# Optimization experiments

Hardware: AMD Instinct MI355X
Metric: run time of the kernel (lower is better)

## Reference

```python
import jax, jax.numpy as jnp
import numpy as np
import math

# config (mirrors FastAttentionConfig)
D_MODEL = 512
D_KEY = 64      # == d_query (required by AbsorptionProjection shape algebra)
D_QUERY = 64
N_HEADS = 8
RANK = 32
RFF_DIM = 128
K_MAX = 64
DIM_GROUPS = [8] * 8  # hyper_cuts_dim_groups, sums to D_KEY
B, L = 2, 2048


def setup_inputs() -> dict:
    key = jax.random.key(0)
    ks = jax.random.split(key, 16)
    r = lambda k, shape, s=1.0: jax.random.normal(k, shape, dtype=jnp.float32) * s
    isr = 1.0 / math.sqrt(RANK)
    return {
        "query": r(ks[0], (B, L, D_MODEL)),
        "key":   r(ks[1], (B, L, D_MODEL)),
        "value": r(ks[2], (B, L, D_MODEL)),
        # down projections (nn.Linear weights stored as (in, out))
        "Wq":  r(ks[3], (D_MODEL, D_QUERY), 0.02), "bq": jnp.zeros((D_QUERY,), jnp.float32),
        "Wkv": r(ks[4], (D_MODEL, D_KEY), 0.02),   "bkv": jnp.zeros((D_KEY,), jnp.float32),
        # per-head absorption projection factors
        "u_q": r(ks[5], (N_HEADS, D_QUERY, RANK), isr), "v_q": r(ks[6], (N_HEADS, RANK, D_KEY), isr),
        "u_k": r(ks[7], (N_HEADS, D_KEY, RANK), isr),   "v_k": r(ks[8], (N_HEADS, RANK, D_KEY), isr),
        # per-head low-rank value up-projection
        "u_v": r(ks[9], (N_HEADS, D_KEY, RANK), isr),   "v_v": r(ks[10], (N_HEADS, RANK, D_MODEL), isr),
        # per-head random Fourier features (frozen params)
        "omega": r(ks[11], (N_HEADS, D_KEY, RFF_DIM)),
        "rff_bias": jax.random.uniform(ks[12], (N_HEADS, RFF_DIM), jnp.float32) * (2.0 * math.pi),
        # output projection
        "W_out": r(ks[13], (N_HEADS * D_MODEL, D_MODEL), 0.02),
        "b_out": jnp.zeros((D_MODEL,), jnp.float32),
    }


def _group_codes(x):
    """Binary-quantize each hyper-cuts dim group and pack bits into one int code per group."""
    codes, start = [], 0
    for gd in DIM_GROUPS:
        bits = (x[..., start:start + gd] > 0).astype(jnp.int32)
        pw = (2 ** jnp.arange(gd, dtype=jnp.int32))
        codes.append(jnp.sum(bits * pw, axis=-1))  # (B, L) int32
        start += gd
    return codes


def _candidates(Qp, K):
    """Wu-Manber prefix match AND Trie full match == exact binary-code match per group
    (prefix_len == group dim). Per group keep first K_MAX matches (ascending index),
    union across groups, sorted ascending, -1-padding handled via mask."""
    Bq, Lq, _ = Qp.shape
    qc, kc = _group_codes(Qp), _group_codes(K)
    union = jnp.zeros((Bq, Lq, Lq), bool)
    for cq, ck in zip(qc, kc):
        m = cq[:, :, None] == ck[:, None, :]                       # (B, L, L)
        keep = m & (jnp.cumsum(m.astype(jnp.int32), axis=-1) <= K_MAX)
        union = union | keep
    idx = jnp.where(union, jnp.arange(Lq, dtype=jnp.int32)[None, None, :], Lq)
    cand = jnp.sort(idx, axis=-1)[:, :, :K_MAX]                    # (B, L, K_MAX)
    mask = cand < Lq
    return jnp.where(mask, cand, 0), mask


def reference(query, key, value, Wq, bq, Wkv, bkv, u_q, v_q, u_k, v_k,
              u_v, v_v, omega, rff_bias, W_out, b_out):
    q_down = query @ Wq + bq          # (B, L, D_QUERY)
    k_down = key @ Wkv + bkv          # (B, L, D_KEY)
    v_down = value @ Wkv + bkv        # (B, L, D_KEY)
    rff_scale = math.sqrt(2.0 / RFF_DIM)
    inv_sqrt = 1.0 / math.sqrt(RFF_DIM)  # optimized_sqrt(RFF_DIM), RFF_DIM is 2^k
    heads = []
    for h in range(N_HEADS):
        # absorption projection: Q into key space
        W_UQ = u_q[h] @ v_q[h]                 # (D_QUERY, D_KEY)
        W_UK = u_k[h] @ v_k[h]                 # (D_KEY, D_KEY)
        W_absorb = W_UK.T @ W_UQ               # (D_KEY, D_QUERY)
        Qp = q_down @ W_absorb.T               # (B, L, D_KEY)
        cand, mask = _candidates(Qp, k_down)
        # RFF-kernelized scores, gathered at candidate positions
        phi_q = jnp.cos(Qp @ omega[h] + rff_bias[h]) * rff_scale     # (B, L, R)
        phi_k = jnp.cos(k_down @ omega[h] + rff_bias[h]) * rff_scale
        scores = jnp.einsum('bir,bjr->bij', phi_q, phi_k) * inv_sqrt  # (B, L, L)
        s = jnp.take_along_axis(scores, cand, axis=2)                 # (B, L, K_MAX)
        s = jnp.where(mask, s, -1e30)
        w = jax.nn.softmax(s, axis=-1) * mask                         # zero invalid slots
        # gather candidate values (d_key space), weighted sum, then low-rank up-proj
        Vc = jnp.take_along_axis(v_down[:, None, :, :], cand[..., None], axis=2)  # (B,L,K,dk)
        ctx = jnp.einsum('blk,blkd->bld', w, Vc)                      # (B, L, D_KEY)
        heads.append(ctx @ (u_v[h] @ v_v[h]))                         # (B, L, D_MODEL)
    concat = jnp.concatenate(heads, axis=-1)                          # (B, L, H*D_MODEL)
    return concat @ W_out + b_out                                     # dropout: eval mode
```

## Files before the change

### kernel.cpp

```cpp
#include <hip/hip_runtime.h>
#include <hip/hip_bf16.h>
#include <math.h>

#define BB 2
#define LL 2048
#define DM 512
#define DK 64
#define NH 8
#define RK 32
#define RFF 128
#define KMAX 64
#define BL (BB*LL)
#define NQ (NH*BB*LL)
#define NCH 16
#define CHW (LL/NCH)

#define RFF_SCALE 0.125f
#define INV_SQRT_RFF 0.08838834764831845f

typedef unsigned long long u64;

__device__ __forceinline__ unsigned int zbytes(unsigned int x) {
  return ~(((x & 0x7F7F7F7Fu) + 0x7F7F7F7Fu) | x | 0x7F7F7F7Fu);
}

__global__ __launch_bounds__(256) void k_down_proj(
    const float* __restrict__ q, const float* __restrict__ k, const float* __restrict__ v,
    const float* __restrict__ Wq, const float* __restrict__ bq,
    const float* __restrict__ Wkv, const float* __restrict__ bkv,
    float* __restrict__ qd, float* __restrict__ kd, float* __restrict__ vd,
    unsigned char* __restrict__ kcodes) {
  int r0 = blockIdx.x * 16;
  int which = blockIdx.y;
  const float* src = (which == 0) ? q : (which == 1) ? k : v;
  const float* W   = (which == 0) ? Wq : Wkv;
  const float* bias= (which == 0) ? bq : bkv;
  float* dst       = (which == 0) ? qd : (which == 1) ? kd : vd;
  int tid = threadIdx.x;
  int d = tid & 63, rg = tid >> 6;

  __shared__ float sin_[16][DM];
  const float4* s4 = (const float4*)(src + (size_t)r0 * DM);
  float4* l4 = (float4*)&sin_[0][0];
  #pragma unroll
  for (int u = 0; u < 8; ++u) l4[tid + u * 256] = s4[tid + u * 256];
  __syncthreads();

  float acc[4] = {0.f, 0.f, 0.f, 0.f};
  for (int t4 = 0; t4 < DM / 4; ++t4) {
    float w[4];
    #pragma unroll
    for (int u = 0; u < 4; ++u) w[u] = W[(t4 * 4 + u) * DK + d];
    #pragma unroll
    for (int r = 0; r < 4; ++r) {
      float4 c4 = *(const float4*)&sin_[rg * 4 + r][t4 * 4];
      acc[r] = fmaf(c4.x, w[0], acc[r]);
      acc[r] = fmaf(c4.y, w[1], acc[r]);
      acc[r] = fmaf(c4.z, w[2], acc[r]);
      acc[r] = fmaf(c4.w, w[3], acc[r]);
    }
  }
  float bs = bias[d];
  #pragma unroll
  for (int r = 0; r < 4; ++r) {
    int R = r0 + rg * 4 + r;
    float val = acc[r] + bs;
    dst[(size_t)R * DK + d] = val;
    if (which == 1) {
      u64 m = __ballot(val > 0.f);
      if (d < 8) {
        int b = R >> 11, j = R & 2047;
        kcodes[(((size_t)b * 8 + d) << 11) + j] = (unsigned char)((m >> (8 * d)) & 0xFF);
      }
    }
  }
}

__global__ __launch_bounds__(256) void k_head_pre(
    const float* __restrict__ u_q, const float* __restrict__ v_q,
    const float* __restrict__ u_k, const float* __restrict__ v_k,
    const float* __restrict__ u_v, const float* __restrict__ v_v,
    float* __restrict__ WabsT, float* __restrict__ Wv) {
  int h = blockIdx.x, tid = threadIdx.x;
  __shared__ float sU[DK * RK];
  __shared__ float sV[RK * DK];
  __shared__ float sWUQ[DK * DK];
  __shared__ float sWUK[DK * DK];
  for (int e = tid; e < DK * RK; e += 256) sU[e] = u_q[h * DK * RK + e];
  for (int e = tid; e < RK * DK; e += 256) sV[e] = v_q[h * RK * DK + e];
  __syncthreads();
  for (int e = tid; e < DK * DK; e += 256) {
    int r = e >> 6, c = e & 63;
    float a = 0.f;
    for (int t = 0; t < RK; ++t) a = fmaf(sU[r * RK + t], sV[t * DK + c], a);
    sWUQ[e] = a;
  }
  __syncthreads();
  for (int e = tid; e < DK * RK; e += 256) sU[e] = u_k[h * DK * RK + e];
  for (int e = tid; e < RK * DK; e += 256) sV[e] = v_k[h * RK * DK + e];
  __syncthreads();
  for (int e = tid; e < DK * DK; e += 256) {
    int r = e >> 6, c = e & 63;
    float a = 0.f;
    for (int t = 0; t < RK; ++t) a = fmaf(sU[r * RK + t], sV[t * DK + c], a);
    sWUK[e] = a;
  }
  __syncthreads();
  for (int e = tid; e < DK * DK; e += 256) {
    int a_ = e >> 6, q_ = e & 63;
    float a = 0.f;
    for (int c = 0; c < DK; ++c) a = fmaf(sWUK[c * DK + a_], sWUQ[c * DK + q_], a);
    WabsT[h * DK * DK + q_ * DK + a_] = a;
  }
  __syncthreads();
  for (int e = tid; e < DK * RK; e += 256) sU[e] = u_v[h * DK * RK + e];
  __syncthreads();
  const float* vv = v_v + (size_t)h * RK * DM;
  for (int e = tid; e < DK * DM; e += 256) {
    int d = e >> 9, o = e & 511;
    float a = 0.f;
    for (int c = 0; c < RK; ++c) a = fmaf(sU[d * RK + c], vv[c * DM + o], a);
    Wv[(size_t)h * DK * DM + e] = a;
  }
}

__global__ __launch_bounds__(256) void k_m2(
    const float* __restrict__ Wv, const float* __restrict__ W_out, float* __restrict__ M2) {
  int h = blockIdx.x, d0 = blockIdx.y * 8;
  int tid = threadIdx.x;
  __shared__ float4 sWv4[8][DM / 4];
  const float4* g4 = (const float4*)(Wv + ((size_t)h * DK + d0) * DM);
  float4* l4 = &sWv4[0][0];
  #pragma unroll
  for (int u = 0; u < 4; ++u) l4[tid + u * 256] = g4[tid + u * 256];
  __syncthreads();
  float a0[8], a1[8];
  #pragma unroll
  for (int r = 0; r < 8; ++r) { a0[r] = 0.f; a1[r] = 0.f; }
  const float* Wo = W_out + (size_t)h * DM * DM;
  for (int p4 = 0; p4 < DM / 4; ++p4) {
    float m0[4], m1[4];
    #pragma unroll
    for (int u = 0; u < 4; ++u) {
      m0[u] = Wo[(size_t)(p4 * 4 + u) * DM + tid];
      m1[u] = Wo[(size_t)(p4 * 4 + u) * DM + tid + 256];
    }
    #pragma unroll
    for (int r = 0; r < 8; ++r) {
      float4 c4 = sWv4[r][p4];
      a0[r] = fmaf(c4.x, m0[0], a0[r]); a0[r] = fmaf(c4.y, m0[1], a0[r]);
      a0[r] = fmaf(c4.z, m0[2], a0[r]); a0[r] = fmaf(c4.w, m0[3], a0[r]);
      a1[r] = fmaf(c4.x, m1[0], a1[r]); a1[r] = fmaf(c4.y, m1[1], a1[r]);
      a1[r] = fmaf(c4.z, m1[2], a1[r]); a1[r] = fmaf(c4.w, m1[3], a1[r]);
    }
  }
  #pragma unroll
  for (int r = 0; r < 8; ++r) {
    size_t row = (size_t)h * DK + d0 + r;
    M2[row * DM + tid] = a0[r];
    M2[row * DM + tid + 256] = a1[r];
  }
}

__global__ __launch_bounds__(256, 4) void k_phi(
    const float* __restrict__ qd, const float* __restrict__ kd,
    const float* __restrict__ WabsT,
    const float* __restrict__ omega, const float* __restrict__ rff_bias,
    float* __restrict__ phiq, float* __restrict__ phik,
    u64* __restrict__ qcodes8) {
  int r0 = blockIdx.x * 16;
  int h = blockIdx.y;
  int isK = blockIdx.z;
  int tid = threadIdx.x;
  __shared__ float sq[16][DK];
  __shared__ float qp[16][DK];

  if (!isK) {
    const float4* g4 = (const float4*)(qd + (size_t)r0 * DK);
    float4* l4 = (float4*)&sq[0][0];
    l4[tid] = g4[tid];
    __syncthreads();
    int a_ = tid & 63, rg = tid >> 6;
    float acc[4] = {0.f, 0.f, 0.f, 0.f};
    const float* Wt = WabsT + h * DK * DK;
    for (int t = 0; t < DK; ++t) {
      float w = Wt[t * DK + a_];
      #pragma unroll
      for (int r = 0; r < 4; ++r) acc[r] = fmaf(sq[rg * 4 + r][t], w, acc[r]);
    }
    #pragma unroll
    for (int r = 0; r < 4; ++r) {
      u64 m = __ballot(acc[r] > 0.f);
      int R = r0 + rg * 4 + r;
      if (a_ == 0) {
        int b = R >> 11, i = R & 2047;
        qcodes8[(((size_t)h * BB + b) << 11) + i] = m;
      }
      qp[R - r0][a_] = acc[r];
    }
    __syncthreads();
  } else {
    const float4* g4 = (const float4*)(kd + (size_t)r0 * DK);
    float4* l4 = (float4*)&qp[0][0];
    l4[tid] = g4[tid];
    __syncthreads();
  }

  int col = tid & 127, rg2 = tid >> 7;
  float acc[8];
  float bias = rff_bias[h * RFF + col];
  #pragma unroll
  for (int r = 0; r < 8; ++r) acc[r] = bias;
  const float* om = omega + (size_t)h * DK * RFF;
  #pragma unroll 4
  for (int d4 = 0; d4 < DK / 4; ++d4) {
    float w[4];
    #pragma unroll
    for (int u = 0; u < 4; ++u) w[u] = om[(size_t)(d4 * 4 + u) * RFF + col];
    #pragma unroll
    for (int r = 0; r < 8; ++r) {
      float4 c4 = *(const float4*)&qp[rg2 * 8 + r][d4 * 4];
      acc[r] = fmaf(c4.x, w[0], acc[r]); acc[r] = fmaf(c4.y, w[1], acc[r]);
      acc[r] = fmaf(c4.z, w[2], acc[r]); acc[r] = fmaf(c4.w, w[3], acc[r]);
    }
  }
  float* dst = isK ? phik : phiq;
  #pragma unroll
  for (int r = 0; r < 8; ++r) {
    int R = r0 + rg2 * 8 + r;
    dst[((size_t)h * BL + R) * RFF + col] = cosf(acc[r]) * RFF_SCALE;
  }
}

__global__ __launch_bounds__(256) void k_bhist(
    const unsigned char* __restrict__ kcodes, int* __restrict__ chist) {
  int bg = blockIdx.x, ch = blockIdx.y;
  int c = threadIdx.x;
  __shared__ unsigned int wrd[CHW / 4];
  if (c < CHW / 4)
    wrd[c] = ((const unsigned int*)(kcodes + (size_t)bg * LL + ch * CHW))[c];
  __syncthreads();
  unsigned int pat = (unsigned)c * 0x01010101u;
  int cnt = 0;
  #pragma unroll
  for (int t = 0; t < CHW / 4; ++t)
    cnt += __popc(zbytes(wrd[t] ^ pat));
  chist[((size_t)bg * NCH + ch) * 256 + c] = cnt;
}

__global__ __launch_bounds__(256) void k_bscan(
    int* __restrict__ chist, int* __restrict__ bcnt) {
  int bg = blockIdx.x, c = threadIdx.x;
  int base = 0;
  #pragma unroll
  for (int ch = 0; ch < NCH; ++ch) {
    size_t idx = ((size_t)bg * NCH + ch) * 256 + c;
    int v = chist[idx];
    chist[idx] = base;
    base += v;
  }
  bcnt[bg * 256 + c] = base < KMAX ? base : KMAX;
}

__global__ __launch_bounds__(256) void k_bscatter(
    const unsigned char* __restrict__ kcodes, const int* __restrict__ chist,
    int* __restrict__ bidx) {
  int bg = blockIdx.x, ch = blockIdx.y;
  int c = threadIdx.x;
  __shared__ unsigned int wrd[CHW / 4];
  if (c < CHW / 4)
    wrd[c] = ((const unsigned int*)(kcodes + (size_t)bg * LL + ch * CHW))[c];
  __syncthreads();
  int pos = chist[((size_t)bg * NCH + ch) * 256 + c];
  if (pos >= KMAX) return;
  unsigned int pat = (unsigned)c * 0x01010101u;
  int* out = bidx + ((size_t)bg * 256 + c) * KMAX;
  int j0 = ch * CHW;
  for (int t = 0; t < CHW / 4; ++t) {
    unsigned int zm = zbytes(wrd[t] ^ pat);
    while (zm) {
      int byte = (__ffs(zm) - 1) >> 3;
      out[pos++] = j0 + t * 4 + byte;
      if (pos >= KMAX) return;
      zm &= zm - 1;
    }
  }
}

__global__ __launch_bounds__(256) void k_attn(
    const u64* __restrict__ qcodes8, const int* __restrict__ bcnt,
    const int* __restrict__ bidx,
    const float* __restrict__ phiq, const float* __restrict__ phik,
    const float* __restrict__ vd, float* __restrict__ ctx) {
  __shared__ __align__(16) int   lcs[4][KMAX];
  __shared__ __align__(16) float lw [4][KMAX];
  __shared__ float        ssc[4][KMAX];
  __shared__ float4       sph[4][RFF / 4];
  __shared__ unsigned int bm [4][64];
  int swz = (blockIdx.x & 7) * ((NQ / 4) / 8) + (blockIdx.x >> 3);
  int lane = threadIdx.x & 63;
  int wv = threadIdx.x >> 6;
  int qidx = swz * 4 + wv;
  int h = qidx >> 12;
  int b = (qidx >> 11) & 1;
  int i = qidx & 2047;
  int base = qidx - i;

  lcs[wv][lane] = 0;
  bm[wv][lane] = 0u;
  u64 qc = qcodes8[(((size_t)h * BB + b) << 11) + i];
  #pragma unroll
  for (int g = 0; g < 8; ++g) {
    int code = (int)((qc >> (8 * g)) & 255);
    int bk = ((b * 8 + g) << 8) + code;
    int cnt = bcnt[bk];
    if (lane < cnt) {
      int j = bidx[(size_t)bk * KMAX + lane];
      atomicOr(&bm[wv][j >> 5], 1u << (j & 31));
    }
  }
  unsigned int wbits = bm[wv][lane];
  int cw = __popc(wbits);
  int pre = cw;
  #pragma unroll
  for (int off = 1; off < 64; off <<= 1) {
    int t = __shfl_up(pre, off);
    if (lane >= off) pre += t;
  }
  int total = __shfl(pre, 63);
  int nv = total < KMAX ? total : KMAX;
  int pos = pre - cw;
  while (wbits && pos < KMAX) {
    int bit = __ffs(wbits) - 1;
    wbits &= wbits - 1;
    lcs[wv][pos++] = (lane << 5) + bit;
  }

  if (lane < RFF / 4)
    sph[wv][lane] = ((const float4*)(phiq + (size_t)qidx * RFF))[lane];

  int k16 = lane >> 2, f = lane & 3;
  #pragma unroll
  for (int cb = 0; cb < 4; ++cb) {
    int cd = cb * 16 + k16;
    int col = lcs[wv][cd];
    const float4* rp = (const float4*)(phik + (size_t)(base + col) * RFF);
    float p = 0.f;
    #pragma unroll
    for (int t = 0; t < 8; ++t) {
      int idx = t * 4 + f;
      float4 kv = rp[idx];
      float4 qv = sph[wv][idx];
      p += kv.x * qv.x + kv.y * qv.y + kv.z * qv.z + kv.w * qv.w;
    }
    p += __shfl_xor(p, 1);
    p += __shfl_xor(p, 2);
    if (f == 0) ssc[wv][cd] = p * INV_SQRT_RFF;
  }

  float s = (lane < nv) ? ssc[wv][lane] : -1e30f;
  float m = s;
  #pragma unroll
  for (int off = 32; off >= 1; off >>= 1) m = fmaxf(m, __shfl_xor(m, off));
  float e = expf(s - m);
  float sum = e;
  #pragma unroll
  for (int off = 32; off >= 1; off >>= 1) sum += __shfl_xor(sum, off);
  float w_ = (lane < nv) ? (e / sum) : 0.f;
  lw[wv][lane] = w_;

  float acc = 0.f;
  const float* vb = vd + (size_t)b * LL * DK;
  for (int k4 = 0; k4 < KMAX / 4; ++k4) {
    float4 w4 = *(const float4*)&lw[wv][k4 * 4];
    int4   c4 = *(const int4*)&lcs[wv][k4 * 4];
    acc = fmaf(w4.x, vb[(size_t)c4.x * DK + lane], acc);
    acc = fmaf(w4.y, vb[(size_t)c4.y * DK + lane], acc);
    acc = fmaf(w4.z, vb[(size_t)c4.z * DK + lane], acc);
    acc = fmaf(w4.w, vb[(size_t)c4.w * DK + lane], acc);
  }
  ctx[((size_t)(b * LL + i)) * (NH * DK) + h * DK + lane] = acc;
}

__global__ __launch_bounds__(256) void k_out(
    const float* __restrict__ ctx, const float* __restrict__ M2,
    const float* __restrict__ b_out, float* __restrict__ out) {
  int r0 = blockIdx.x * 16;
  int tid = threadIdx.x;
  __shared__ float4 sctx4[16][DM / 4];
  const float4* g4 = (const float4*)(ctx + (size_t)r0 * DM);
  float4* l4 = &sctx4[0][0];
  #pragma unroll
  for (int u = 0; u < 8; ++u) l4[tid + u * 256] = g4[tid + u * 256];
  __syncthreads();
  float a0[16], a1[16];
  #pragma unroll
  for (int r = 0; r < 16; ++r) { a0[r] = 0.f; a1[r] = 0.f; }
  for (int p4 = 0; p4 < DM / 4; ++p4) {
    float m0[4], m1[4];
    #pragma unroll
    for (int u = 0; u < 4; ++u) {
      m0[u] = M2[(size_t)(p4 * 4 + u) * DM + tid];
      m1[u] = M2[(size_t)(p4 * 4 + u) * DM + tid + 256];
    }
    #pragma unroll
    for (int r = 0; r < 16; ++r) {
      float4 c4 = sctx4[r][p4];
      a0[r] = fmaf(c4.x, m0[0], a0[r]); a0[r] = fmaf(c4.y, m0[1], a0[r]);
      a0[r] = fmaf(c4.z, m0[2], a0[r]); a0[r] = fmaf(c4.w, m0[3], a0[r]);
      a1[r] = fmaf(c4.x, m1[0], a1[r]); a1[r] = fmaf(c4.y, m1[1], a1[r]);
      a1[r] = fmaf(c4.z, m1[2], a1[r]); a1[r] = fmaf(c4.w, m1[3], a1[r]);
    }
  }
  float b0 = b_out[tid], b1 = b_out[tid + 256];
  #pragma unroll
  for (int r = 0; r < 16; ++r) {
    out[(size_t)(r0 + r) * DM + tid] = a0[r] + b0;
    out[(size_t)(r0 + r) * DM + tid + 256] = a1[r] + b1;
  }
}

extern "C" void kernel_launch(void* const* d_in, const int* in_sizes, int n_in,
                              void* d_out, int out_size, void* d_ws, size_t ws_size,
                              hipStream_t stream) {
  const float* query = (const float*)d_in[0];
  const float* key   = (const float*)d_in[1];
  const float* value = (const float*)d_in[2];
  const float* Wq    = (const float*)d_in[3];
  const float* bq    = (const float*)d_in[4];
  const float* Wkv   = (const float*)d_in[5];
  const float* bkv   = (const float*)d_in[6];
  const float* u_q   = (const float*)d_in[7];
  const float* v_q   = (const float*)d_in[8];
  const float* u_k   = (const float*)d_in[9];
  const float* v_k   = (const float*)d_in[10];
  const float* u_v   = (const float*)d_in[11];
  const float* v_v   = (const float*)d_in[12];
  const float* omega = (const float*)d_in[13];
  const float* rffb  = (const float*)d_in[14];
  const float* W_out = (const float*)d_in[15];
  const float* b_out = (const float*)d_in[16];
  float* out = (float*)d_out;

  size_t off = 0;
  char* ws = (char*)d_ws;
  auto carve = [&](size_t bytes) -> void* {
    void* p = ws + off;
    off += (bytes + 255) & ~(size_t)255;
    return p;
  };
  float* qd    = (float*)carve((size_t)BL * DK * 4);
  float* kd    = (float*)carve((size_t)BL * DK * 4);
  float* vd    = (float*)carve((size_t)BL * DK * 4);
  float* WabsT = (float*)carve((size_t)NH * DK * DK * 4);
  float* Wv    = (float*)carve((size_t)NH * DK * DM * 4);
  float* M2    = (float*)carve((size_t)NH * DK * DM * 4);
  float* phiq  = (float*)carve((size_t)NQ * RFF * 4);
  float* phik  = (float*)carve((size_t)NQ * RFF * 4);
  unsigned char* kcodes = (unsigned char*)carve((size_t)BB * 8 * LL);
  u64* qcodes8 = (u64*)carve((size_t)NH * BB * LL * 8);
  int* chist = (int*)carve((size_t)BB * 8 * NCH * 256 * 4);
  int* bcnt  = (int*)carve((size_t)BB * 8 * 256 * 4);
  int* bidx  = (int*)carve((size_t)BB * 8 * 256 * KMAX * 4);
  float* ctx = (float*)carve((size_t)BL * NH * DK * 4);
  (void)ws_size;

  k_down_proj<<<dim3(BL / 16, 3), 256, 0, stream>>>(query, key, value, Wq, bq, Wkv, bkv,
                                                    qd, kd, vd, kcodes);
  k_head_pre<<<NH, 256, 0, stream>>>(u_q, v_q, u_k, v_k, u_v, v_v, WabsT, Wv);
  k_m2<<<dim3(NH, 8), 256, 0, stream>>>(Wv, W_out, M2);
  k_phi<<<dim3(BL / 16, NH, 2), 256, 0, stream>>>(qd, kd, WabsT, omega, rffb,
                                                  phiq, phik, qcodes8);
  k_bhist<<<dim3(BB * 8, NCH), 256, 0, stream>>>(kcodes, chist);
  k_bscan<<<BB * 8, 256, 0, stream>>>(chist, bcnt);
  k_bscatter<<<dim3(BB * 8, NCH), 256, 0, stream>>>(kcodes, chist, bidx);
  k_attn<<<NQ / 4, 256, 0, stream>>>(qcodes8, bcnt, bidx, phiq, phik, vd, ctx);
  k_out<<<BL / 16, 256, 0, stream>>>(ctx, M2, b_out, out);
}
```

Before: 522.9 us.

## Enlarge k_phi row tile to 64 and stage omega in shared memory

k_phi now handles 64 rows per block instead of 16 and loads the per-head omega matrix into shared memory once per block. Each thread keeps 16 or 32 row accumulators, so every omega and WabsT value is reused more often and global reads drop. Outputs are written with nontemporal stores. The larger shared footprint (about 64KB) and higher register use lower occupancy, and the grid shrinks to 1024 blocks.

Measured after the change: 430.7 us. -17.6%, faster.

```diff
diff --git a/kernel.cpp b/kernel.cpp
--- a/kernel.cpp
+++ b/kernel.cpp
@@ -162,74 +162,81 @@
   }
 }
 
-__global__ __launch_bounds__(256, 4) void k_phi(
+__global__ __launch_bounds__(256, 2) void k_phi(
     const float* __restrict__ qd, const float* __restrict__ kd,
     const float* __restrict__ WabsT,
     const float* __restrict__ omega, const float* __restrict__ rff_bias,
     float* __restrict__ phiq, float* __restrict__ phik,
     u64* __restrict__ qcodes8) {
-  int r0 = blockIdx.x * 16;
+  int r0 = blockIdx.x * 64;
   int h = blockIdx.y;
   int isK = blockIdx.z;
   int tid = threadIdx.x;
-  __shared__ float sq[16][DK];
-  __shared__ float qp[16][DK];
+  __shared__ float som[DK][RFF];
+  __shared__ float qp[64][DK];
+  __shared__ float sq[64][DK];
+
+  const float4* og = (const float4*)(omega + (size_t)h * DK * RFF);
+  float4* o4 = (float4*)&som[0][0];
+  #pragma unroll
+  for (int u = 0; u < 8; ++u) o4[tid + u * 256] = og[tid + u * 256];
 
   if (!isK) {
     const float4* g4 = (const float4*)(qd + (size_t)r0 * DK);
     float4* l4 = (float4*)&sq[0][0];
-    l4[tid] = g4[tid];
+    #pragma unroll
+    for (int u = 0; u < 4; ++u) l4[tid + u * 256] = g4[tid + u * 256];
     __syncthreads();
-    int a_ = tid & 63, rg = tid >> 6;
-    float acc[4] = {0.f, 0.f, 0.f, 0.f};
+    int a_ = tid & 63, wv = tid >> 6;
+    float acc[16];
+    #pragma unroll
+    for (int r = 0; r < 16; ++r) acc[r] = 0.f;
     const float* Wt = WabsT + h * DK * DK;
     for (int t = 0; t < DK; ++t) {
       float w = Wt[t * DK + a_];
       #pragma unroll
-      for (int r = 0; r < 4; ++r) acc[r] = fmaf(sq[rg * 4 + r][t], w, acc[r]);
-    }
-    #pragma unroll
-    for (int r = 0; r < 4; ++r) {
+      for (int r = 0; r < 16; ++r) acc[r] = fmaf(sq[wv * 16 + r][t], w, acc[r]);
+    }
+    #pragma unroll
+    for (int r = 0; r < 16; ++r) {
       u64 m = __ballot(acc[r] > 0.f);
-      int R = r0 + rg * 4 + r;
+      int R = r0 + wv * 16 + r;
       if (a_ == 0) {
         int b = R >> 11, i = R & 2047;
         qcodes8[(((size_t)h * BB + b) << 11) + i] = m;
       }
-      qp[R - r0][a_] = acc[r];
+      qp[wv * 16 + r][a_] = acc[r];
     }
     __syncthreads();
   } else {
     const float4* g4 = (const float4*)(kd + (size_t)r0 * DK);
     float4* l4 = (float4*)&qp[0][0];
-    l4[tid] = g4[tid];
+    #pragma unroll
+    for (int u = 0; u < 4; ++u) l4[tid + u * 256] = g4[tid + u * 256];
     __syncthreads();
   }
 
-  int col = tid & 127, rg2 = tid >> 7;
-  float acc[8];
+  int col = tid & 127, half = tid >> 7;
   float bias = rff_bias[h * RFF + col];
-  #pragma unroll
-  for (int r = 0; r < 8; ++r) acc[r] = bias;
-  const float* om = omega + (size_t)h * DK * RFF;
-  #pragma unroll 4
+  float acc2[32];
+  #pragma unroll
+  for (int r = 0; r < 32; ++r) acc2[r] = bias;
   for (int d4 = 0; d4 < DK / 4; ++d4) {
     float w[4];
     #pragma unroll
-    for (int u = 0; u < 4; ++u) w[u] = om[(size_t)(d4 * 4 + u) * RFF + col];
-    #pragma unroll
-    for (int r = 0; r < 8; ++r) {
-      float4 c4 = *(const float4*)&qp[rg2 * 8 + r][d4 * 4];
-      acc[r] = fmaf(c4.x, w[0], acc[r]); acc[r] = fmaf(c4.y, w[1], acc[r]);
-      acc[r] = fmaf(c4.z, w[2], acc[r]); acc[r] = fmaf(c4.w, w[3], acc[r]);
-    }
-  }
-  float* dst = isK ? phik : phiq;
-  #pragma unroll
-  for (int r = 0; r < 8; ++r) {
-    int R = r0 + rg2 * 8 + r;
-    dst[((size_t)h * BL + R) * RFF + col] = cosf(acc[r]) * RFF_SCALE;
-  }
+    for (int u = 0; u < 4; ++u) w[u] = som[d4 * 4 + u][col];
+    #pragma unroll
+    for (int r = 0; r < 32; ++r) {
+      float4 qv = *(const float4*)&qp[half * 32 + r][d4 * 4];
+      acc2[r] = fmaf(qv.x, w[0], acc2[r]); acc2[r] = fmaf(qv.y, w[1], acc2[r]);
+      acc2[r] = fmaf(qv.z, w[2], acc2[r]); acc2[r] = fmaf(qv.w, w[3], acc2[r]);
+    }
+  }
+  float* dst = (isK ? phik : phiq) +
+               ((size_t)h * BL + r0 + half * 32) * RFF + col;
+  #pragma unroll
+  for (int r = 0; r < 32; ++r)
+    __builtin_nontemporal_store(cosf(acc2[r]) * RFF_SCALE, dst + (size_t)r * RFF);
 }
 
 __global__ __launch_bounds__(256) void k_bhist(
@@ -469,7 +476,7 @@
                                                     qd, kd, vd, kcodes);
   k_head_pre<<<NH, 256, 0, stream>>>(u_q, v_q, u_k, v_k, u_v, v_v, WabsT, Wv);
   k_m2<<<dim3(NH, 8), 256, 0, stream>>>(Wv, W_out, M2);
-  k_phi<<<dim3(BL / 16, NH, 2), 256, 0, stream>>>(qd, kd, WabsT, omega, rffb,
+  k_phi<<<dim3(BL / 64, NH, 2), 256, 0, stream>>>(qd, kd, WabsT, omega, rffb,
                                                   phiq, phik, qcodes8);
   k_bhist<<<dim3(BB * 8, NCH), 256, 0, stream>>>(kcodes, chist);
   k_bscan<<<BB * 8, 256, 0, stream>>>(chist, bcnt);
```
